# Kernel tuning notes

Hardware: AMD Instinct MI355X
Metric: run time of the kernel (lower is better)

## Reference

```python
import jax, jax.numpy as jnp
import numpy as np
from jax import lax

T, B, D, H = 256, 32, 768, 768


def setup_inputs() -> dict:
    key = jax.random.key(0)
    ks = jax.random.split(key, 8)
    s = 1.0 / np.sqrt(H)
    x = jax.random.normal(ks[0], (T, B, D), dtype=jnp.float32)
    h0 = jax.random.normal(ks[1], (2, B, H), dtype=jnp.float32) * s
    wih_f = jax.random.normal(ks[2], (3 * H, D), dtype=jnp.float32) * s
    whh_f = jax.random.normal(ks[3], (3 * H, H), dtype=jnp.float32) * s
    wih_b = jax.random.normal(ks[4], (3 * H, D), dtype=jnp.float32) * s
    whh_b = jax.random.normal(ks[5], (3 * H, H), dtype=jnp.float32) * s
    bih_f = jnp.zeros((3 * H,), jnp.float32)
    bhh_f = jnp.zeros((3 * H,), jnp.float32)
    bih_b = jnp.zeros((3 * H,), jnp.float32)
    bhh_b = jnp.zeros((3 * H,), jnp.float32)
    # sorted-descending lengths in [T//2, T], as PackedSequence requires
    lengths = jnp.sort(jax.random.randint(ks[6], (B,), T // 2, T + 1))[::-1].astype(jnp.int32)
    return dict(x=x, h0=h0, wih_f=wih_f, whh_f=whh_f, bih_f=bih_f, bhh_f=bhh_f,
                wih_b=wih_b, whh_b=whh_b, bih_b=bih_b, bhh_b=bhh_b, lengths=lengths)


def _gru_scan(x_seq, h0d, Wih, Whh, bih, bhh, mask):
    """Masked GRU scan. x_seq [T,B,D], mask [T,B] bool; hidden frozen where mask is False
    (equivalent to PackedSequence shrinking/growing the active batch)."""
    def step(h, inp):
        x_t, m = inp  # [B,D], [B]
        gx = x_t @ Wih.T + bih          # [B,3H]
        gh = h @ Whh.T + bhh            # [B,3H]
        xr, xz, xn = jnp.split(gx, 3, axis=-1)
        hr, hz, hn = jnp.split(gh, 3, axis=-1)
        r = jax.nn.sigmoid(xr + hr)
        z = jax.nn.sigmoid(xz + hz)
        n = jnp.tanh(xn + r * hn)
        h_new = (1.0 - z) * n + z * h
        h_new = jnp.where(m[:, None], h_new, h)
        return h_new, h_new * m[:, None]  # zero outputs at padded positions
    h_last, outs = lax.scan(step, h0d, (x_seq, mask))
    return outs, h_last


def reference(x, h0, wih_f, whh_f, bih_f, bhh_f, wih_b, whh_b, bih_b, bhh_b, lengths):
    t_idx = jnp.arange(T)[:, None]                 # [T,1]
    mask = t_idx < lengths[None, :]                # [T,B]
    # forward direction
    out_f, h_f = _gru_scan(x, h0[0], wih_f, whh_f, bih_f, bhh_f, mask)
    # reverse direction: flip time, run, flip back
    out_b_rev, h_b = _gru_scan(x[::-1], h0[1], wih_b, whh_b, bih_b, bhh_b, mask[::-1])
    out_b = out_b_rev[::-1]
    outputs = jnp.concatenate([out_f, out_b], axis=-1)  # [T,B,2H], zero beyond length
    h_out = jnp.stack([h_f, h_b], axis=0)                # [2,B,H]
    return outputs, h_out
```

## Files before the change

kernel.cpp:

```cpp
#include <hip/hip_runtime.h>
#include <stdint.h>

typedef unsigned short u16;
typedef unsigned int u32;
typedef _Float16 f16;
typedef __attribute__((ext_vector_type(2))) __fp16 h16x2;
typedef __attribute__((ext_vector_type(8))) _Float16 f16x8;
typedef __attribute__((ext_vector_type(4))) float f32x4;
typedef __attribute__((ext_vector_type(4))) unsigned short u16x4;
typedef __attribute__((ext_vector_type(4))) unsigned int u32x4;

#define T_SEQ  256
#define BATCH  32
#define DIM    768
#define HID    768
#define G3     2304
#define N_ALL  4608
#define NSLICE 48
#define NBLK   96
#define FLAG_STRIDE 32

__device__ __forceinline__ u16 f2h(float f) {
  return __builtin_bit_cast(u16, (f16)f);
}
__device__ __forceinline__ float h2f(u16 h) {
  return (float)__builtin_bit_cast(f16, h);
}

__device__ __forceinline__ f16x8 load_coh16(const u16* p) {
  f16x8 v;
  asm volatile("global_load_dwordx4 %0, %1, off sc0 sc1" : "=v"(v) : "v"(p));
  return v;
}
__device__ __forceinline__ void store_coh16(u16* p, f16x8 v) {
  asm volatile("global_store_dwordx4 %0, %1, off sc0 sc1" :: "v"(p), "v"(v));
}
__device__ __forceinline__ void wait_vm0() {
  asm volatile("s_waitcnt vmcnt(0)" ::: "memory");
}
__device__ __forceinline__ u32 pkrtz(float a, float b) {
  h16x2 p = __builtin_amdgcn_cvt_pkrtz(a, b);
  return __builtin_bit_cast(u32, p);
}
__device__ __forceinline__ f16x8 cvt8(float4 a, float4 b) {
  u32x4 r;
  r.x = pkrtz(a.x, a.y);
  r.y = pkrtz(a.z, a.w);
  r.z = pkrtz(b.x, b.y);
  r.w = pkrtz(b.z, b.w);
  return __builtin_bit_cast(f16x8, r);
}

__global__ void k_cvt(const float* __restrict__ in, u16* __restrict__ out, int n4) {
  int i = blockIdx.x * blockDim.x + threadIdx.x;
  if (i >= n4) return;
  float4 v = ((const float4*)in)[i];
  u16x4 o;
  o[0] = f2h(v.x); o[1] = f2h(v.y); o[2] = f2h(v.z); o[3] = f2h(v.w);
  ((u16x4*)out)[i] = o;
}

__global__ __launch_bounds__(256) void k_gemm(
    const float* __restrict__ X, const float* __restrict__ Wf,
    const float* __restrict__ Wb,
    const float* __restrict__ bihf, const float* __restrict__ bihb,
    u16* __restrict__ gx)
{
  __shared__ __align__(16) u16 As[128 * 32];
  __shared__ __align__(16) u16 Bs[128 * 32];
  const int tid  = threadIdx.x;
  const int lane = tid & 63, wave = tid >> 6;
  const int wm = wave >> 1, wn = wave & 1;
  const int m0 = blockIdx.y * 128;
  const int n0 = blockIdx.x * 128;
  const int lr = lane & 15, lk = lane >> 4;
  f32x4 acc[4][4] = {};
  for (int k0 = 0; k0 < DIM; k0 += 32) {
    __syncthreads();
    #pragma unroll
    for (int i = 0; i < 2; ++i) {
      int cidx = i * 256 + tid;
      int row = cidx >> 2, kk = (cidx & 3) * 8;
      const float* ap = &X[(size_t)(m0 + row) * DIM + k0 + kk];
      *(f16x8*)&As[cidx * 8] = cvt8(*(const float4*)ap, *(const float4*)(ap + 4));
      int n = n0 + row;
      const float* bp = (n < G3 ? &Wf[(size_t)n * DIM] : &Wb[(size_t)(n - G3) * DIM]) + k0 + kk;
      *(f16x8*)&Bs[cidx * 8] = cvt8(*(const float4*)bp, *(const float4*)(bp + 4));
    }
    __syncthreads();
    f16x8 af[4], bfr[4];
    #pragma unroll
    for (int f = 0; f < 4; ++f) {
      af[f]  = *(const f16x8*)&As[(wm * 64 + f * 16 + lr) * 32 + lk * 8];
      bfr[f] = *(const f16x8*)&Bs[(wn * 64 + f * 16 + lr) * 32 + lk * 8];
    }
    #pragma unroll
    for (int fm = 0; fm < 4; ++fm)
      #pragma unroll
      for (int fn = 0; fn < 4; ++fn)
        acc[fm][fn] = __builtin_amdgcn_mfma_f32_16x16x32_f16(af[fm], bfr[fn], acc[fm][fn], 0, 0, 0);
  }
  #pragma unroll
  for (int fm = 0; fm < 4; ++fm)
    #pragma unroll
    for (int fn = 0; fn < 4; ++fn) {
      int n = n0 + wn * 64 + fn * 16 + lr;
      float bias = (n < G3) ? bihf[n] : bihb[n - G3];
      #pragma unroll
      for (int r = 0; r < 4; ++r) {
        int m = m0 + wm * 64 + fm * 16 + lk * 4 + r;
        gx[(size_t)m * N_ALL + n] = f2h(acc[fm][fn][r] + bias);
      }
    }
}

__global__ __launch_bounds__(256, 1) void k_gru(
    const u16* __restrict__ whh,
    const u16* __restrict__ gx,
    const float* __restrict__ h0,
    const float* __restrict__ bhhf, const float* __restrict__ bhhb,
    const int* __restrict__ lengths,
    u16* __restrict__ hbuf,
    float* __restrict__ out, int* __restrict__ flags)
{
  const int blk   = blockIdx.x;
  const int dir   = blk / NSLICE;
  const int slice = blk % NSLICE;
  const int hbase = slice * 16;
  const int tid = threadIdx.x, lane = tid & 63, wave = tid >> 6;
  const int lr = lane & 15, lk = lane >> 4;
  const int c = hbase + lr;
  const int pollid = tid - 128;
  __shared__ __align__(16) float part[3][2][3][64][4];
  __shared__ __align__(16) u16 hx[32][16];

  f16x8 bw[3][6];
  #pragma unroll
  for (int g = 0; g < 3; ++g)
    #pragma unroll
    for (int ks = 0; ks < 6; ++ks)
      bw[g][ks] = *(const f16x8*)&whh[(size_t)(dir * G3 + g * HID + hbase + lr) * HID
                                      + wave * 192 + ks * 32 + lk * 8];

  float hst[2][4];
  float bh[3] = {0.f, 0.f, 0.f};
  int lenv[2][4];
  u16 g0[2][4], g1[2][4], g2[2][4];
  if (wave == 0) {
    #pragma unroll
    for (int m = 0; m < 2; ++m)
      #pragma unroll
      for (int r = 0; r < 4; ++r) {
        int b = m * 16 + lk * 4 + r;
        float h = h0[(size_t)dir * BATCH * HID + (size_t)b * HID + c];
        hst[m][r] = h;
        lenv[m][r] = lengths[b];
        hx[b][lr] = f2h(h);
      }
    const float* bhp = dir ? bhhb : bhhf;
    #pragma unroll
    for (int g = 0; g < 3; ++g) bh[g] = bhp[g * HID + c];
    asm volatile("s_waitcnt lgkmcnt(0)" ::: "memory");
    {
      f16x8 hv = *(const f16x8*)&hx[lane >> 1][(lane & 1) * 8];
      store_coh16(&hbuf[(size_t)(dir * BATCH + (lane >> 1)) * HID + hbase + (lane & 1) * 8], hv);
    }
    wait_vm0();
    if (lane == 0)
      __hip_atomic_store(&flags[blk * FLAG_STRIDE], 1, __ATOMIC_RELAXED, __HIP_MEMORY_SCOPE_AGENT);
    int t0 = dir ? (T_SEQ - 1) : 0;
    #pragma unroll
    for (int m = 0; m < 2; ++m)
      #pragma unroll
      for (int r = 0; r < 4; ++r) {
        int b = m * 16 + lk * 4 + r;
        size_t off = ((size_t)t0 * BATCH + b) * N_ALL + dir * G3 + c;
        g0[m][r] = gx[off]; g1[m][r] = gx[off + HID]; g2[m][r] = gx[off + 2 * HID];
      }
    wait_vm0();
  }
  if (pollid >= 0 && pollid < NSLICE) {
    const int watch = (dir * NSLICE + pollid) * FLAG_STRIDE;
    while (__hip_atomic_load(&flags[watch], __ATOMIC_RELAXED, __HIP_MEMORY_SCOPE_AGENT) < 1)
      __builtin_amdgcn_s_sleep(1);
  }
  __syncthreads();

  for (int s = 0; s < T_SEQ; ++s) {
    const int par = s & 1;
    const int t = dir ? (T_SEQ - 1 - s) : s;
    const u16* hb = hbuf + (size_t)(par * 2 + dir) * BATCH * HID;
    f16x8 ah[2][6];
    #pragma unroll
    for (int m = 0; m < 2; ++m)
      #pragma unroll
      for (int ks = 0; ks < 6; ++ks)
        ah[m][ks] = load_coh16(&hb[(size_t)(m * 16 + lr) * HID + wave * 192 + ks * 32 + lk * 8]);
    wait_vm0();
    __builtin_amdgcn_sched_barrier(0);
    f32x4 acc[2][3] = {};
    #pragma unroll
    for (int ks = 0; ks < 6; ++ks)
      #pragma unroll
      for (int m = 0; m < 2; ++m)
        #pragma unroll
        for (int g = 0; g < 3; ++g)
          acc[m][g] = __builtin_amdgcn_mfma_f32_16x16x32_f16(ah[m][ks], bw[g][ks], acc[m][g], 0, 0, 0);
    if (wave != 0) {
      #pragma unroll
      for (int m = 0; m < 2; ++m)
        #pragma unroll
        for (int g = 0; g < 3; ++g)
          *(f32x4*)&part[wave - 1][m][g][lane][0] = acc[m][g];
    }
    __syncthreads();
    if (wave == 0) {
      u16* hbn = hbuf + (size_t)((par ^ 1) * 2 + dir) * BATCH * HID;
      float outv[2][4];
      #pragma unroll
      for (int m = 0; m < 2; ++m) {
        f32x4 gh[3];
        #pragma unroll
        for (int g = 0; g < 3; ++g) {
          f32x4 v = acc[m][g];
          #pragma unroll
          for (int w = 0; w < 3; ++w) v += *(const f32x4*)&part[w][m][g][lane][0];
          gh[g] = v;
        }
        #pragma unroll
        for (int r = 0; r < 4; ++r) {
          int b = m * 16 + lk * 4 + r;
          float xr = h2f(g0[m][r]), xz = h2f(g1[m][r]), xn = h2f(g2[m][r]);
          float rg = 1.f / (1.f + __expf(-(xr + gh[0][r] + bh[0])));
          float zg = 1.f / (1.f + __expf(-(xz + gh[1][r] + bh[1])));
          float e2 = __expf(2.f * (xn + rg * (gh[2][r] + bh[2])));
          float ng = 1.f - 2.f / (e2 + 1.f);
          float hp = hst[m][r];
          bool msk = t < lenv[m][r];
          float hn = msk ? ((1.f - zg) * ng + zg * hp) : hp;
          hst[m][r] = hn;
          outv[m][r] = msk ? hn : 0.f;
          hx[b][lr] = f2h(hn);
        }
      }
      asm volatile("s_waitcnt lgkmcnt(0)" ::: "memory");
      {
        f16x8 hv = *(const f16x8*)&hx[lane >> 1][(lane & 1) * 8];
        store_coh16(&hbn[(size_t)(lane >> 1) * HID + hbase + (lane & 1) * 8], hv);
      }
      wait_vm0();
      if (lane == 0)
        __hip_atomic_store(&flags[blk * FLAG_STRIDE], s + 2, __ATOMIC_RELAXED, __HIP_MEMORY_SCOPE_AGENT);
      #pragma unroll
      for (int m = 0; m < 2; ++m)
        #pragma unroll
        for (int r = 0; r < 4; ++r) {
          int b = m * 16 + lk * 4 + r;
          __builtin_nontemporal_store(outv[m][r],
              &out[((size_t)t * BATCH + b) * (2 * HID) + (size_t)dir * HID + c]);
        }
      if (s + 1 < T_SEQ) {
        int t2 = dir ? (T_SEQ - 2 - s) : (s + 1);
        #pragma unroll
        for (int m = 0; m < 2; ++m)
          #pragma unroll
          for (int r = 0; r < 4; ++r) {
            int b = m * 16 + lk * 4 + r;
            size_t off = ((size_t)t2 * BATCH + b) * N_ALL + dir * G3 + c;
            g0[m][r] = gx[off]; g1[m][r] = gx[off + HID]; g2[m][r] = gx[off + 2 * HID];
          }
      }
      wait_vm0();
    }
    if (pollid >= 0 && pollid < NSLICE) {
      const int watch = (dir * NSLICE + pollid) * FLAG_STRIDE;
      while (__hip_atomic_load(&flags[watch], __ATOMIC_RELAXED, __HIP_MEMORY_SCOPE_AGENT) < s + 2)
        __builtin_amdgcn_s_sleep(1);
    }
    __syncthreads();
  }
  if (wave == 0) {
    #pragma unroll
    for (int m = 0; m < 2; ++m)
      #pragma unroll
      for (int r = 0; r < 4; ++r) {
        int b = m * 16 + lk * 4 + r;
        out[(size_t)T_SEQ * BATCH * 2 * HID + (size_t)dir * BATCH * HID + (size_t)b * HID + c] = hst[m][r];
      }
  }
}

extern "C" void kernel_launch(void* const* d_in, const int* in_sizes, int n_in,
                              void* d_out, int out_size, void* d_ws, size_t ws_size,
                              hipStream_t stream) {
  const float* x     = (const float*)d_in[0];
  const float* h0    = (const float*)d_in[1];
  const float* wihf  = (const float*)d_in[2];
  const float* whhf  = (const float*)d_in[3];
  const float* bihf  = (const float*)d_in[4];
  const float* bhhf  = (const float*)d_in[5];
  const float* wihb  = (const float*)d_in[6];
  const float* whhb  = (const float*)d_in[7];
  const float* bihb  = (const float*)d_in[8];
  const float* bhhb  = (const float*)d_in[9];
  const int* lengths = (const int*)d_in[10];
  float* out = (float*)d_out;
  char* ws = (char*)d_ws;

  int* flags = (int*)(ws + 0);
  u16* whh_h = (u16*)(ws + 24576);
  u16* hbuf  = (u16*)(ws + 7102464);
  u16* gx    = (u16*)(ws + 7299072);

  k_cvt<<<1728, 256, 0, stream>>>(whhf, whh_h,            442368);
  k_cvt<<<1728, 256, 0, stream>>>(whhb, whh_h + 1769472,  442368);
  (void)hipMemsetAsync(flags, 0, NBLK * FLAG_STRIDE * sizeof(int), stream);
  k_gemm<<<dim3(36, 64), 256, 0, stream>>>(x, wihf, wihb, bihf, bihb, gx);
  k_gru<<<NBLK, 256, 0, stream>>>(whh_h, gx, h0, bhhf, bhhb, lengths, hbuf, out, flags);
}
```

Measured before the change: 1.301 ms.

## Dedicate a producer wave to gx prefetch, output stores and flag polling

The recurrent matmul now runs on three waves (K split 3x256 instead of 4x192), and the fourth wave becomes a helper. It prefetches the next step's input gates into double-buffered LDS, writes the previous step's outputs from an LDS buffer, and polls the neighbour flags. This takes global gx loads and output stores off the critical wave-0 path after the hidden-state publish. In exchange, each MFMA wave carries more K work and registers, which may lengthen the per-step matmul.

```diff
diff --git a/kernel.cpp b/kernel.cpp
--- a/kernel.cpp
+++ b/kernel.cpp
@@ -130,23 +130,30 @@
   const int tid = threadIdx.x, lane = tid & 63, wave = tid >> 6;
   const int lr = lane & 15, lk = lane >> 4;
   const int c = hbase + lr;
-  const int pollid = tid - 128;
-  __shared__ __align__(16) float part[3][2][3][64][4];
+  const int cc = lane & 15, bq = lane >> 4;
+
+  __shared__ __align__(16) float part[2][2][3][64][4];
+  __shared__ __align__(16) u16 gxl[2][3][32][16];
+  __shared__ __align__(16) float outb[2][32][16];
   __shared__ __align__(16) u16 hx[32][16];
 
-  f16x8 bw[3][6];
-  #pragma unroll
-  for (int g = 0; g < 3; ++g)
-    #pragma unroll
-    for (int ks = 0; ks < 6; ++ks)
-      bw[g][ks] = *(const f16x8*)&whh[(size_t)(dir * G3 + g * HID + hbase + lr) * HID
-                                      + wave * 192 + ks * 32 + lk * 8];
+  f16x8 bw[3][8];
+  if (wave < 3) {
+    #pragma unroll
+    for (int g = 0; g < 3; ++g)
+      #pragma unroll
+      for (int ks = 0; ks < 8; ++ks)
+        bw[g][ks] = *(const f16x8*)&whh[(size_t)(dir * G3 + g * HID + hbase + lr) * HID
+                                        + wave * 256 + ks * 32 + lk * 8];
+  }
 
   float hst[2][4];
   float bh[3] = {0.f, 0.f, 0.f};
   int lenv[2][4];
-  u16 g0[2][4], g1[2][4], g2[2][4];
   if (wave == 0) {
+    const float* bhp = dir ? bhhb : bhhf;
+    #pragma unroll
+    for (int g = 0; g < 3; ++g) bh[g] = bhp[g * HID + c];
     #pragma unroll
     for (int m = 0; m < 2; ++m)
       #pragma unroll
@@ -157,9 +164,6 @@
         lenv[m][r] = lengths[b];
         hx[b][lr] = f2h(h);
       }
-    const float* bhp = dir ? bhhb : bhhf;
-    #pragma unroll
-    for (int g = 0; g < 3; ++g) bh[g] = bhp[g * HID + c];
     asm volatile("s_waitcnt lgkmcnt(0)" ::: "memory");
     {
       f16x8 hv = *(const f16x8*)&hx[lane >> 1][(lane & 1) * 8];
@@ -168,55 +172,75 @@
     wait_vm0();
     if (lane == 0)
       __hip_atomic_store(&flags[blk * FLAG_STRIDE], 1, __ATOMIC_RELAXED, __HIP_MEMORY_SCOPE_AGENT);
+  } else if (wave == 3) {
     int t0 = dir ? (T_SEQ - 1) : 0;
     #pragma unroll
-    for (int m = 0; m < 2; ++m)
-      #pragma unroll
-      for (int r = 0; r < 4; ++r) {
-        int b = m * 16 + lk * 4 + r;
-        size_t off = ((size_t)t0 * BATCH + b) * N_ALL + dir * G3 + c;
-        g0[m][r] = gx[off]; g1[m][r] = gx[off + HID]; g2[m][r] = gx[off + 2 * HID];
-      }
-    wait_vm0();
-  }
-  if (pollid >= 0 && pollid < NSLICE) {
-    const int watch = (dir * NSLICE + pollid) * FLAG_STRIDE;
-    while (__hip_atomic_load(&flags[watch], __ATOMIC_RELAXED, __HIP_MEMORY_SCOPE_AGENT) < 1)
-      __builtin_amdgcn_s_sleep(1);
+    for (int g = 0; g < 3; ++g)
+      #pragma unroll
+      for (int j = 0; j < 8; ++j) {
+        int b = bq * 8 + j;
+        gxl[0][g][b][cc] = gx[((size_t)t0 * BATCH + b) * N_ALL + dir * G3 + g * HID + hbase + cc];
+      }
+    if (lane < NSLICE) {
+      const int watch = (dir * NSLICE + lane) * FLAG_STRIDE;
+      while (__hip_atomic_load(&flags[watch], __ATOMIC_RELAXED, __HIP_MEMORY_SCOPE_AGENT) < 1)
+        __builtin_amdgcn_s_sleep(1);
+    }
   }
   __syncthreads();
 
   for (int s = 0; s < T_SEQ; ++s) {
     const int par = s & 1;
     const int t = dir ? (T_SEQ - 1 - s) : s;
-    const u16* hb = hbuf + (size_t)(par * 2 + dir) * BATCH * HID;
-    f16x8 ah[2][6];
-    #pragma unroll
-    for (int m = 0; m < 2; ++m)
-      #pragma unroll
-      for (int ks = 0; ks < 6; ++ks)
-        ah[m][ks] = load_coh16(&hb[(size_t)(m * 16 + lr) * HID + wave * 192 + ks * 32 + lk * 8]);
-    wait_vm0();
-    __builtin_amdgcn_sched_barrier(0);
     f32x4 acc[2][3] = {};
-    #pragma unroll
-    for (int ks = 0; ks < 6; ++ks)
-      #pragma unroll
-      for (int m = 0; m < 2; ++m)
+    u16 gpre[24];
+    if (wave < 3) {
+      const u16* hb = hbuf + (size_t)(par * 2 + dir) * BATCH * HID;
+      f16x8 ah[2][8];
+      #pragma unroll
+      for (int m2 = 0; m2 < 2; ++m2)
+        #pragma unroll
+        for (int ks = 0; ks < 8; ++ks)
+          ah[m2][ks] = load_coh16(&hb[(size_t)(m2 * 16 + lr) * HID + wave * 256 + ks * 32 + lk * 8]);
+      wait_vm0();
+      __builtin_amdgcn_sched_barrier(0);
+      #pragma unroll
+      for (int ks = 0; ks < 8; ++ks)
+        #pragma unroll
+        for (int m2 = 0; m2 < 2; ++m2)
+          #pragma unroll
+          for (int g = 0; g < 3; ++g)
+            acc[m2][g] = __builtin_amdgcn_mfma_f32_16x16x32_f16(ah[m2][ks], bw[g][ks], acc[m2][g], 0, 0, 0);
+      if (wave != 0) {
+        #pragma unroll
+        for (int m2 = 0; m2 < 2; ++m2)
+          #pragma unroll
+          for (int g = 0; g < 3; ++g)
+            *(f32x4*)&part[wave - 1][m2][g][lane][0] = acc[m2][g];
+      }
+    } else {
+      if (s + 1 < T_SEQ) {
+        int t2 = dir ? (T_SEQ - 2 - s) : (s + 1);
         #pragma unroll
         for (int g = 0; g < 3; ++g)
-          acc[m][g] = __builtin_amdgcn_mfma_f32_16x16x32_f16(ah[m][ks], bw[g][ks], acc[m][g], 0, 0, 0);
-    if (wave != 0) {
-      #pragma unroll
-      for (int m = 0; m < 2; ++m)
-        #pragma unroll
-        for (int g = 0; g < 3; ++g)
-          *(f32x4*)&part[wave - 1][m][g][lane][0] = acc[m][g];
+          #pragma unroll
+          for (int j = 0; j < 8; ++j)
+            gpre[g * 8 + j] = gx[((size_t)t2 * BATCH + bq * 8 + j) * N_ALL
+                                 + dir * G3 + g * HID + hbase + cc];
+      }
+      if (s > 0) {
+        int tprev = dir ? (T_SEQ - s) : (s - 1);
+        #pragma unroll
+        for (int j = 0; j < 8; ++j) {
+          float v = outb[par ^ 1][bq * 8 + j][cc];
+          __builtin_nontemporal_store(v,
+              &out[((size_t)tprev * BATCH + bq * 8 + j) * (2 * HID) + (size_t)dir * HID + hbase + cc]);
+        }
+      }
     }
     __syncthreads();
     if (wave == 0) {
       u16* hbn = hbuf + (size_t)((par ^ 1) * 2 + dir) * BATCH * HID;
-      float outv[2][4];
       #pragma unroll
       for (int m = 0; m < 2; ++m) {
         f32x4 gh[3];
@@ -224,13 +248,15 @@
         for (int g = 0; g < 3; ++g) {
           f32x4 v = acc[m][g];
           #pragma unroll
-          for (int w = 0; w < 3; ++w) v += *(const f32x4*)&part[w][m][g][lane][0];
+          for (int w = 0; w < 2; ++w) v += *(const f32x4*)&part[w][m][g][lane][0];
           gh[g] = v;
         }
         #pragma unroll
         for (int r = 0; r < 4; ++r) {
           int b = m * 16 + lk * 4 + r;
-          float xr = h2f(g0[m][r]), xz = h2f(g1[m][r]), xn = h2f(g2[m][r]);
+          float xr = h2f(gxl[par][0][b][lr]);
+          float xz = h2f(gxl[par][1][b][lr]);
+          float xn = h2f(gxl[par][2][b][lr]);
           float rg = 1.f / (1.f + __expf(-(xr + gh[0][r] + bh[0])));
           float zg = 1.f / (1.f + __expf(-(xz + gh[1][r] + bh[1])));
           float e2 = __expf(2.f * (xn + rg * (gh[2][r] + bh[2])));
@@ -239,7 +265,7 @@
           bool msk = t < lenv[m][r];
           float hn = msk ? ((1.f - zg) * ng + zg * hp) : hp;
           hst[m][r] = hn;
-          outv[m][r] = msk ? hn : 0.f;
+          outb[par][b][lr] = msk ? hn : 0.f;
           hx[b][lr] = f2h(hn);
         }
       }
@@ -251,31 +277,19 @@
       wait_vm0();
       if (lane == 0)
         __hip_atomic_store(&flags[blk * FLAG_STRIDE], s + 2, __ATOMIC_RELAXED, __HIP_MEMORY_SCOPE_AGENT);
-      #pragma unroll
-      for (int m = 0; m < 2; ++m)
-        #pragma unroll
-        for (int r = 0; r < 4; ++r) {
-          int b = m * 16 + lk * 4 + r;
-          __builtin_nontemporal_store(outv[m][r],
-              &out[((size_t)t * BATCH + b) * (2 * HID) + (size_t)dir * HID + c]);
-        }
+    } else if (wave == 3) {
       if (s + 1 < T_SEQ) {
-        int t2 = dir ? (T_SEQ - 2 - s) : (s + 1);
-        #pragma unroll
-        for (int m = 0; m < 2; ++m)
-          #pragma unroll
-          for (int r = 0; r < 4; ++r) {
-            int b = m * 16 + lk * 4 + r;
-            size_t off = ((size_t)t2 * BATCH + b) * N_ALL + dir * G3 + c;
-            g0[m][r] = gx[off]; g1[m][r] = gx[off + HID]; g2[m][r] = gx[off + 2 * HID];
-          }
-      }
-      wait_vm0();
-    }
-    if (pollid >= 0 && pollid < NSLICE) {
-      const int watch = (dir * NSLICE + pollid) * FLAG_STRIDE;
-      while (__hip_atomic_load(&flags[watch], __ATOMIC_RELAXED, __HIP_MEMORY_SCOPE_AGENT) < s + 2)
-        __builtin_amdgcn_s_sleep(1);
+        #pragma unroll
+        for (int g = 0; g < 3; ++g)
+          #pragma unroll
+          for (int j = 0; j < 8; ++j)
+            gxl[par ^ 1][g][bq * 8 + j][cc] = gpre[g * 8 + j];
+      }
+      if (lane < NSLICE) {
+        const int watch = (dir * NSLICE + lane) * FLAG_STRIDE;
+        while (__hip_atomic_load(&flags[watch], __ATOMIC_RELAXED, __HIP_MEMORY_SCOPE_AGENT) < s + 2)
+          __builtin_amdgcn_s_sleep(1);
+      }
     }
     __syncthreads();
   }
@@ -287,6 +301,14 @@
         int b = m * 16 + lk * 4 + r;
         out[(size_t)T_SEQ * BATCH * 2 * HID + (size_t)dir * BATCH * HID + (size_t)b * HID + c] = hst[m][r];
       }
+  } else if (wave == 3) {
+    int tlast = dir ? 0 : (T_SEQ - 1);
+    #pragma unroll
+    for (int j = 0; j < 8; ++j) {
+      float v = outb[(T_SEQ - 1) & 1][bq * 8 + j][cc];
+      __builtin_nontemporal_store(v,
+          &out[((size_t)tlast * BATCH + bq * 8 + j) * (2 * HID) + (size_t)dir * HID + hbase + cc]);
+    }
   }
 }
 
```

After: 1.389 ms. 1.07x slower.
